# Performance work log

Measured on AMD Instinct MI355X. Metric: run time of the kernel, lower is better.

## Reference

```python
import jax, jax.numpy as jnp
import numpy as np

NUM_EXPERTS = 8
EMBED_DIM = 1024
BATCH, SEQ = 4, 2048


def setup_inputs() -> dict:
    key = jax.random.key(0)
    k1, k2, k3 = jax.random.split(key, 3)
    E_symb = jax.random.normal(k1, (BATCH, SEQ, EMBED_DIM), dtype=jnp.float32)
    gate_w = jax.random.normal(k2, (EMBED_DIM, NUM_EXPERTS), dtype=jnp.float32) * 0.02
    gate_b = jnp.zeros((NUM_EXPERTS,), dtype=jnp.float32)
    expert_w = jax.random.normal(k3, (NUM_EXPERTS, EMBED_DIM, EMBED_DIM), dtype=jnp.float32) * 0.02
    return {"E_symb": E_symb, "gate_w": gate_w, "gate_b": gate_b,
            "expert_w": expert_w, "k": 2}


def reference(E_symb, gate_w, gate_b, expert_w, k):
    B, S, D = E_symb.shape
    E = expert_w.shape[0]
    x = E_symb.reshape(-1, D)                       # [T, D]
    logits = x @ gate_w + gate_b                    # [T, E]
    probs = jax.nn.softmax(logits.astype(jnp.float32), axis=-1)
    # top-k selection; NOTE: original renormalizes routing_weights but never
    # applies them to expert outputs -> combine is an UNWEIGHTED sum.
    _, sel = jax.lax.top_k(probs, k)                # [T, k]
    mask = jax.nn.one_hot(sel, E, dtype=x.dtype).sum(axis=1)  # [T, E] in {0,1}
    # dense grouped-GEMM then masked combine (replaces per-expert gather/scatter loop)
    y = jnp.einsum('td,edf->tef', x, expert_w)      # [T, E, D]
    out = jnp.einsum('tef,te->tf', y, mask)         # [T, D]
    return out.reshape(B, S, D)
```

## Files before the change

kernel.cpp:

```cpp
#include <hip/hip_runtime.h>
#include <hip/hip_bf16.h>
#include <stdint.h>

#define T_TOK 8192
#define DIM   1024
#define NEXP  8
#define BM    128
#define BN    128
#define BK    64

typedef __bf16 bf16_t;
typedef bf16_t bf16x8 __attribute__((ext_vector_type(8)));
typedef bf16_t bf16x4 __attribute__((ext_vector_type(4)));
typedef float  f32x4  __attribute__((ext_vector_type(4)));

#define WS_CNT    0
#define CIDX(p)   ((p) << 4)
#define WS_LIST   8192
#define WS_XBF    (4u << 20)
#define WS_W2     (20u << 20)
#define WS_NEED_PSUM ((size_t)76 << 20)

__device__ const int d_PA[28] = {0,0,0,0,0,0,0,1,1,1,1,1,1,2,2,2,2,2,3,3,3,3,4,4,4,5,5,6};
__device__ const int d_PB[28] = {1,2,3,4,5,6,7,2,3,4,5,6,7,3,4,5,6,7,4,5,6,7,5,6,7,6,7,7};

__device__ __forceinline__ void gload16(const void* g, void* l) {
    __builtin_amdgcn_global_load_lds(
        (const __attribute__((address_space(1))) unsigned int*)g,
        (__attribute__((address_space(3))) unsigned int*)l, 16, 0, 0);
}

__device__ __forceinline__ int swz(int r, int k) {
    return ((r * BK + k) * 2) ^ ((r & 7) << 4);
}

#define WAITCNT_VM0()   do { asm volatile("s_waitcnt vmcnt(0)" ::: "memory"); \
                             __builtin_amdgcn_sched_barrier(0); } while (0)
#define WAITCNT_VM8()   do { asm volatile("s_waitcnt vmcnt(8)" ::: "memory"); \
                             __builtin_amdgcn_sched_barrier(0); } while (0)
#define WAITCNT_LGKM0() do { asm volatile("s_waitcnt lgkmcnt(0)" ::: "memory"); \
                             __builtin_amdgcn_sched_barrier(0); } while (0)
#define BARRIER()       do { __builtin_amdgcn_s_barrier(); \
                             __builtin_amdgcn_sched_barrier(0); } while (0)

template <int PSUM>
__global__ __launch_bounds__(256) void fused_pre(const float* __restrict__ x,
                                                 const float* __restrict__ gw,
                                                 const float* __restrict__ gb,
                                                 const float* __restrict__ ew,
                                                 bf16_t* __restrict__ xbf,
                                                 bf16_t* __restrict__ w2,
                                                 int* __restrict__ cnt,
                                                 int* __restrict__ list) {
    __shared__ __align__(16) float sh[NEXP * DIM];
    int bx  = blockIdx.x;
    int tid = threadIdx.x;
    if (bx < 1024) {
        float4 gb0 = *(const float4*)gb;
        float4 gb1 = *(const float4*)(gb + 4);
        float gbl[8] = {gb0.x, gb0.y, gb0.z, gb0.w, gb1.x, gb1.y, gb1.z, gb1.w};
        float* gwt = sh;
        const float4* gw4 = (const float4*)gw;
        #pragma unroll
        for (int i = 0; i < 8; i++) {
            int f4 = tid + i * 256;
            float4 v = gw4[f4];
            int d  = f4 >> 1;
            int e0 = (f4 & 1) * 4;
            gwt[(e0 + 0) * DIM + d] = v.x;
            gwt[(e0 + 1) * DIM + d] = v.y;
            gwt[(e0 + 2) * DIM + d] = v.z;
            gwt[(e0 + 3) * DIM + d] = v.w;
        }
        __syncthreads();
        int wid  = tid >> 6;
        int lane = tid & 63;
        const float4* gwt4 = (const float4*)gwt;
        for (int tt = 0; tt < 2; tt++) {
            int t = bx * 8 + wid * 2 + tt;
            const float4* xr4 = (const float4*)(x + (size_t)t * DIM);
            float acc[NEXP] = {};
            #pragma unroll
            for (int j = 0; j < 4; j++) {
                int c4 = j * 64 + lane;
                float4 v = xr4[c4];
                bf16x4 b;
                b[0] = (bf16_t)v.x; b[1] = (bf16_t)v.y;
                b[2] = (bf16_t)v.z; b[3] = (bf16_t)v.w;
                *(bf16x4*)(xbf + (size_t)t * DIM + c4 * 4) = b;
                #pragma unroll
                for (int e = 0; e < NEXP; e++) {
                    float4 g = gwt4[e * 256 + c4];
                    acc[e] += v.x * g.x + v.y * g.y + v.z * g.z + v.w * g.w;
                }
            }
            for (int off = 32; off >= 1; off >>= 1)
                #pragma unroll
                for (int e = 0; e < NEXP; e++)
                    acc[e] += __shfl_xor(acc[e], off, 64);
            if (lane == 0) {
                float logit[NEXP];
                #pragma unroll
                for (int e = 0; e < NEXP; e++) logit[e] = acc[e] + gbl[e];
                int b1 = 0; float best = logit[0];
                for (int e = 1; e < NEXP; e++) if (logit[e] > best) { best = logit[e]; b1 = e; }
                int b2 = -1; float best2 = -3.0e38f;
                for (int e = 0; e < NEXP; e++) {
                    if (e == b1) continue;
                    if (logit[e] > best2) { best2 = logit[e]; b2 = e; }
                }
                int a = min(b1, b2), bb = max(b1, b2);
                int p = a * 8 + bb;
                int pos = atomicAdd(&cnt[CIDX(p)], 1);
                list[p * T_TOK + pos] = t;
            }
        }
    } else {
        int bz  = bx - 1024;
        int g   = bz >> 8;
        int rem = bz & 255;
        int f0  = (rem & 15) * 64;
        int d0  = (rem >> 4) * 64;
        float (*tile)[65] = (float (*)[65])sh;
        int a = PSUM ? d_PA[g] : g;
        int b = PSUM ? d_PB[g] : g;
        const float* s1 = ew + ((size_t)a * DIM + d0) * DIM + f0;
        const float* s2 = ew + ((size_t)b * DIM + d0) * DIM + f0;
        int fl = (tid & 15) * 4;
        int dl = tid >> 4;
        #pragma unroll
        for (int i = 0; i < 4; i++) {
            int d = dl + i * 16;
            float4 u = *(const float4*)(s1 + (size_t)d * DIM + fl);
            if (PSUM) {
                float4 v = *(const float4*)(s2 + (size_t)d * DIM + fl);
                u.x += v.x; u.y += v.y; u.z += v.z; u.w += v.w;
            }
            tile[d][fl + 0] = u.x; tile[d][fl + 1] = u.y;
            tile[d][fl + 2] = u.z; tile[d][fl + 3] = u.w;
        }
        __syncthreads();
        bf16_t* dst = w2 + ((size_t)g * DIM + f0) * DIM + d0;
        int dl2 = (tid & 7) * 8;
        int fl2 = tid >> 3;
        #pragma unroll
        for (int i = 0; i < 2; i++) {
            int f = fl2 + i * 32;
            bf16x8 o;
            #pragma unroll
            for (int c = 0; c < 8; c++) o[c] = (bf16_t)tile[dl2 + c][f];
            *(bf16x8*)(dst + (size_t)f * DIM + dl2) = o;
        }
    }
}

template <int PSUM>
__global__ __launch_bounds__(256, 2) void moe_gemm(const bf16_t* __restrict__ xbf,
                                                   const bf16_t* __restrict__ wsrc,
                                                   const int* __restrict__ cnt,
                                                   const int* __restrict__ list,
                                                   float* __restrict__ out) {
    __shared__ __align__(16) bf16_t As[2][BM * BK];
    __shared__ __align__(16) bf16_t Bs[2][BN * BK];
    __shared__ int toks[BM];
    __shared__ int s_desc[128];
    __shared__ int s_ntile;
    int tid  = threadIdx.x;
    int lane = tid & 63;
    int wv   = tid >> 6;
    int wm   = wv >> 1, wn = wv & 1;

    if (tid < 64) {
        int c  = cnt[CIDX(tid)];
        int tp = (c + BM - 1) >> 7;
        int pre = 0, tot = 0;
        for (int i = 0; i < 64; i++) {
            int v = __shfl(tp, i, 64);
            if (i < tid) pre += v;
            tot += v;
        }
        for (int j = 0; j < tp; j++)
            s_desc[pre + j] = tid | ((j * BM) << 8);
        if (tid == 0) s_ntile = tot;
    }
    __syncthreads();
    int nwork = s_ntile * (DIM / BN);
    int vb = ((blockIdx.x & 7) << 6) | (blockIdx.x >> 3);

    for (int wi = 0; wi < 2; wi++) {
        int w = vb * 2 + wi;
        if (w >= nwork) break;
        __syncthreads();
        int dsc = s_desc[w >> 3];
        int n0  = (w & 7) * BN;
        int p   = dsc & 63;
        int m0  = dsc >> 8;
        int e1  = p >> 3, e2 = p & 7;
        int cp  = cnt[CIDX(p)];
        int valid = min(BM, cp - m0);
        if (tid < BM) toks[tid] = list[p * T_TOK + m0 + min(tid, valid - 1)];
        __syncthreads();

        const bf16_t* asrc[4];
        #pragma unroll
        for (int i = 0; i < 4; i++) {
            int c = i * 256 + tid;
            int r = c >> 3, js = (c & 7) ^ (r & 7);
            asrc[i] = xbf + (size_t)toks[r] * DIM + js * 8;
        }

        f32x4 acc[4][4] = {};
        int lr = lane & 15;
        int lk = (lane >> 4) * 8;

        if (PSUM) {
            const bf16_t* bsrc[4];
            int pk = e1 * 7 - (e1 * (e1 - 1)) / 2 + (e2 - e1 - 1);
            const bf16_t* bb = wsrc + (size_t)pk * DIM * DIM;
            #pragma unroll
            for (int i = 0; i < 4; i++) {
                int c = i * 256 + tid;
                int r = c >> 3, js = (c & 7) ^ (r & 7);
                bsrc[i] = bb + (size_t)(n0 + r) * DIM + js * 8;
            }
            #pragma unroll
            for (int i = 0; i < 4; i++)
                gload16(asrc[i], &As[0][(i * 256 + wv * 64) * 8]);
            #pragma unroll
            for (int i = 0; i < 4; i++)
                gload16(bsrc[i], &Bs[0][(i * 256 + wv * 64) * 8]);

            for (int ks = 0; ks < DIM / BK; ks++) {
                int cur = ks & 1;
                if (ks < DIM / BK - 1) {
                    int k1 = (ks + 1) * BK;
                    #pragma unroll
                    for (int i = 0; i < 4; i++)
                        gload16(asrc[i] + k1, &As[cur ^ 1][(i * 256 + wv * 64) * 8]);
                    #pragma unroll
                    for (int i = 0; i < 4; i++)
                        gload16(bsrc[i] + k1, &Bs[cur ^ 1][(i * 256 + wv * 64) * 8]);
                    WAITCNT_VM8();
                } else {
                    WAITCNT_VM0();
                }
                BARRIER();
                const char* Ab = (const char*)As[cur];
                const char* Bb = (const char*)Bs[cur];
                bf16x8 af[2][4], bfr[2][4];
                #pragma unroll
                for (int kk = 0; kk < 2; kk++) {
                    #pragma unroll
                    for (int mf = 0; mf < 4; mf++)
                        af[kk][mf] = *(const bf16x8*)(Ab + swz(wm * 64 + mf * 16 + lr, kk * 32 + lk));
                    #pragma unroll
                    for (int nf = 0; nf < 4; nf++)
                        bfr[kk][nf] = *(const bf16x8*)(Bb + swz(wn * 64 + nf * 16 + lr, kk * 32 + lk));
                }
                #pragma unroll
                for (int kk = 0; kk < 2; kk++)
                    #pragma unroll
                    for (int mf = 0; mf < 4; mf++)
                        #pragma unroll
                        for (int nf = 0; nf < 4; nf++)
                            acc[mf][nf] = __builtin_amdgcn_mfma_f32_16x16x32_bf16(
                                af[kk][mf], bfr[kk][nf], acc[mf][nf], 0, 0, 0);
                BARRIER();
            }
        } else {
            const bf16_t* wt1 = wsrc + (size_t)e1 * DIM * DIM;
            const bf16_t* wt2 = wsrc + (size_t)e2 * DIM * DIM;
            for (int ks = 0; ks < DIM / BK; ks++) {
                int k0 = ks * BK;
                #pragma unroll
                for (int i = 0; i < 4; i++)
                    gload16(asrc[i] + k0, &As[0][(i * 256 + wv * 64) * 8]);
                #pragma unroll
                for (int fo = 0; fo < 2; fo++) {
                    int f = fo * 64 + (tid >> 2), q = tid & 3;
                    const bf16_t* s1 = wt1 + (size_t)(n0 + f) * DIM + k0 + q * 16;
                    const bf16_t* s2 = wt2 + (size_t)(n0 + f) * DIM + k0 + q * 16;
                    bf16x8 u0 = *(const bf16x8*)s1, u1 = *(const bf16x8*)(s1 + 8);
                    bf16x8 w0 = *(const bf16x8*)s2, w1 = *(const bf16x8*)(s2 + 8);
                    bf16x8 o0, o1;
                    #pragma unroll
                    for (int i = 0; i < 8; i++) {
                        o0[i] = (bf16_t)((float)u0[i] + (float)w0[i]);
                        o1[i] = (bf16_t)((float)u1[i] + (float)w1[i]);
                    }
                    *(bf16x8*)((char*)Bs[0] + swz(f, q * 16))     = o0;
                    *(bf16x8*)((char*)Bs[0] + swz(f, q * 16 + 8)) = o1;
                }
                WAITCNT_LGKM0();
                WAITCNT_VM0();
                BARRIER();
                const char* Ab = (const char*)As[0];
                const char* Bb = (const char*)Bs[0];
                bf16x8 af[2][4], bfr[2][4];
                #pragma unroll
                for (int kk = 0; kk < 2; kk++) {
                    #pragma unroll
                    for (int mf = 0; mf < 4; mf++)
                        af[kk][mf] = *(const bf16x8*)(Ab + swz(wm * 64 + mf * 16 + lr, kk * 32 + lk));
                    #pragma unroll
                    for (int nf = 0; nf < 4; nf++)
                        bfr[kk][nf] = *(const bf16x8*)(Bb + swz(wn * 64 + nf * 16 + lr, kk * 32 + lk));
                }
                #pragma unroll
                for (int kk = 0; kk < 2; kk++)
                    #pragma unroll
                    for (int mf = 0; mf < 4; mf++)
                        #pragma unroll
                        for (int nf = 0; nf < 4; nf++)
                            acc[mf][nf] = __builtin_amdgcn_mfma_f32_16x16x32_bf16(
                                af[kk][mf], bfr[kk][nf], acc[mf][nf], 0, 0, 0);
                BARRIER();
            }
        }

        #pragma unroll
        for (int mf = 0; mf < 4; mf++) {
            #pragma unroll
            for (int reg = 0; reg < 4; reg++) {
                int rl = wm * 64 + mf * 16 + (lane >> 4) * 4 + reg;
                if (rl < valid) {
                    size_t trow = (size_t)toks[rl] * DIM;
                    #pragma unroll
                    for (int nf = 0; nf < 4; nf++)
                        out[trow + n0 + wn * 64 + nf * 16 + lr] = acc[mf][nf][reg];
                }
            }
        }
    }
}

extern "C" void kernel_launch(void* const* d_in, const int* in_sizes, int n_in,
                              void* d_out, int out_size, void* d_ws, size_t ws_size,
                              hipStream_t stream) {
    const float* x  = (const float*)d_in[0];
    const float* gw = (const float*)d_in[1];
    const float* gb = (const float*)d_in[2];
    const float* ew = (const float*)d_in[3];
    float* out = (float*)d_out;
    char* ws = (char*)d_ws;
    int*    cnt  = (int*)(ws + WS_CNT);
    int*    list = (int*)(ws + WS_LIST);
    bf16_t* xbf  = (bf16_t*)(ws + WS_XBF);
    bf16_t* w2   = (bf16_t*)(ws + WS_W2);
    bool psum = (ws_size >= WS_NEED_PSUM);

    hipMemsetAsync(d_ws, 0, 8192, stream);
    if (psum) {
        fused_pre<1><<<dim3(1024 + 28 * 256), 256, 0, stream>>>(x, gw, gb, ew,
                                                                xbf, w2, cnt, list);
        moe_gemm<1><<<dim3(512), 256, 0, stream>>>(xbf, w2, cnt, list, out);
    } else {
        fused_pre<0><<<dim3(1024 + 8 * 256), 256, 0, stream>>>(x, gw, gb, ew,
                                                               xbf, w2, cnt, list);
        moe_gemm<0><<<dim3(512), 256, 0, stream>>>(xbf, w2, cnt, list, out);
    }
}
```

Before: 82.37 us.

## Halve GEMM K-tile, one tile per block, raise occupancy to four blocks

The grouped MoE GEMM moves from a 64-wide K tile to a 32-wide one, which halves shared memory per block and adjusts the swizzle to match. Launch bounds rise from 2 to 4 blocks per CU. The grid doubles to 1024 blocks, each handling a single output tile instead of looping over two. The aim is more resident waves to hide global-to-LDS latency and better load balance, at the cost of twice as many K iterations with barriers and less MFMA work per barrier.

```diff
diff --git a/kernel.cpp b/kernel.cpp
--- a/kernel.cpp
+++ b/kernel.cpp
@@ -7,7 +7,7 @@
 #define NEXP  8
 #define BM    128
 #define BN    128
-#define BK    64
+#define BK2   32
 
 typedef __bf16 bf16_t;
 typedef bf16_t bf16x8 __attribute__((ext_vector_type(8)));
@@ -30,13 +30,13 @@
         (__attribute__((address_space(3))) unsigned int*)l, 16, 0, 0);
 }
 
-__device__ __forceinline__ int swz(int r, int k) {
-    return ((r * BK + k) * 2) ^ ((r & 7) << 4);
+__device__ __forceinline__ int swz32(int r, int k) {
+    return ((r * BK2 + k) * 2) ^ (((r >> 1) & 3) << 4);
 }
 
 #define WAITCNT_VM0()   do { asm volatile("s_waitcnt vmcnt(0)" ::: "memory"); \
                              __builtin_amdgcn_sched_barrier(0); } while (0)
-#define WAITCNT_VM8()   do { asm volatile("s_waitcnt vmcnt(8)" ::: "memory"); \
+#define WAITCNT_VM4()   do { asm volatile("s_waitcnt vmcnt(4)" ::: "memory"); \
                              __builtin_amdgcn_sched_barrier(0); } while (0)
 #define WAITCNT_LGKM0() do { asm volatile("s_waitcnt lgkmcnt(0)" ::: "memory"); \
                              __builtin_amdgcn_sched_barrier(0); } while (0)
@@ -155,13 +155,13 @@
 }
 
 template <int PSUM>
-__global__ __launch_bounds__(256, 2) void moe_gemm(const bf16_t* __restrict__ xbf,
+__global__ __launch_bounds__(256, 4) void moe_gemm(const bf16_t* __restrict__ xbf,
                                                    const bf16_t* __restrict__ wsrc,
                                                    const int* __restrict__ cnt,
                                                    const int* __restrict__ list,
                                                    float* __restrict__ out) {
-    __shared__ __align__(16) bf16_t As[2][BM * BK];
-    __shared__ __align__(16) bf16_t Bs[2][BN * BK];
+    __shared__ __align__(16) bf16_t As[2][BM * BK2];
+    __shared__ __align__(16) bf16_t Bs[2][BN * BK2];
     __shared__ int toks[BM];
     __shared__ int s_desc[128];
     __shared__ int s_ntile;
@@ -185,150 +185,131 @@
     }
     __syncthreads();
     int nwork = s_ntile * (DIM / BN);
-    int vb = ((blockIdx.x & 7) << 6) | (blockIdx.x >> 3);
-
-    for (int wi = 0; wi < 2; wi++) {
-        int w = vb * 2 + wi;
-        if (w >= nwork) break;
-        __syncthreads();
-        int dsc = s_desc[w >> 3];
-        int n0  = (w & 7) * BN;
-        int p   = dsc & 63;
-        int m0  = dsc >> 8;
-        int e1  = p >> 3, e2 = p & 7;
-        int cp  = cnt[CIDX(p)];
-        int valid = min(BM, cp - m0);
-        if (tid < BM) toks[tid] = list[p * T_TOK + m0 + min(tid, valid - 1)];
-        __syncthreads();
-
-        const bf16_t* asrc[4];
-        #pragma unroll
-        for (int i = 0; i < 4; i++) {
+    int vb = ((blockIdx.x & 7) << 7) | (blockIdx.x >> 3);
+    if (vb >= nwork) return;
+
+    int dsc = s_desc[vb >> 3];
+    int n0  = (vb & 7) * BN;
+    int p   = dsc & 63;
+    int m0  = dsc >> 8;
+    int e1  = p >> 3, e2 = p & 7;
+    int cp  = cnt[CIDX(p)];
+    int valid = min(BM, cp - m0);
+    if (tid < BM) toks[tid] = list[p * T_TOK + m0 + min(tid, valid - 1)];
+    __syncthreads();
+
+    const bf16_t* asrc[2];
+    #pragma unroll
+    for (int i = 0; i < 2; i++) {
+        int c = i * 256 + tid;
+        int r = c >> 2, js = (c & 3) ^ ((r >> 1) & 3);
+        asrc[i] = xbf + (size_t)toks[r] * DIM + js * 8;
+    }
+
+    f32x4 acc[4][4] = {};
+    int lr = lane & 15;
+    int lk = (lane >> 4) * 8;
+
+    if (PSUM) {
+        const bf16_t* bsrc[2];
+        int pk = e1 * 7 - (e1 * (e1 - 1)) / 2 + (e2 - e1 - 1);
+        const bf16_t* bb = wsrc + (size_t)pk * DIM * DIM;
+        #pragma unroll
+        for (int i = 0; i < 2; i++) {
             int c = i * 256 + tid;
-            int r = c >> 3, js = (c & 7) ^ (r & 7);
-            asrc[i] = xbf + (size_t)toks[r] * DIM + js * 8;
-        }
-
-        f32x4 acc[4][4] = {};
-        int lr = lane & 15;
-        int lk = (lane >> 4) * 8;
-
-        if (PSUM) {
-            const bf16_t* bsrc[4];
-            int pk = e1 * 7 - (e1 * (e1 - 1)) / 2 + (e2 - e1 - 1);
-            const bf16_t* bb = wsrc + (size_t)pk * DIM * DIM;
-            #pragma unroll
-            for (int i = 0; i < 4; i++) {
+            int r = c >> 2, js = (c & 3) ^ ((r >> 1) & 3);
+            bsrc[i] = bb + (size_t)(n0 + r) * DIM + js * 8;
+        }
+        #pragma unroll
+        for (int i = 0; i < 2; i++)
+            gload16(asrc[i], &As[0][(i * 256 + wv * 64) * 8]);
+        #pragma unroll
+        for (int i = 0; i < 2; i++)
+            gload16(bsrc[i], &Bs[0][(i * 256 + wv * 64) * 8]);
+
+        for (int ks = 0; ks < DIM / BK2; ks++) {
+            int cur = ks & 1;
+            if (ks < DIM / BK2 - 1) {
+                int k1 = (ks + 1) * BK2;
+                #pragma unroll
+                for (int i = 0; i < 2; i++)
+                    gload16(asrc[i] + k1, &As[cur ^ 1][(i * 256 + wv * 64) * 8]);
+                #pragma unroll
+                for (int i = 0; i < 2; i++)
+                    gload16(bsrc[i] + k1, &Bs[cur ^ 1][(i * 256 + wv * 64) * 8]);
+                WAITCNT_VM4();
+            } else {
+                WAITCNT_VM0();
+            }
+            BARRIER();
+            const char* Ab = (const char*)As[cur];
+            const char* Bb = (const char*)Bs[cur];
+            bf16x8 af[4], bfr[4];
+            #pragma unroll
+            for (int mf = 0; mf < 4; mf++)
+                af[mf] = *(const bf16x8*)(Ab + swz32(wm * 64 + mf * 16 + lr, lk));
+            #pragma unroll
+            for (int nf = 0; nf < 4; nf++)
+                bfr[nf] = *(const bf16x8*)(Bb + swz32(wn * 64 + nf * 16 + lr, lk));
+            #pragma unroll
+            for (int mf = 0; mf < 4; mf++)
+                #pragma unroll
+                for (int nf = 0; nf < 4; nf++)
+                    acc[mf][nf] = __builtin_amdgcn_mfma_f32_16x16x32_bf16(
+                        af[mf], bfr[nf], acc[mf][nf], 0, 0, 0);
+            BARRIER();
+        }
+    } else {
+        const bf16_t* wt1 = wsrc + (size_t)e1 * DIM * DIM;
+        const bf16_t* wt2 = wsrc + (size_t)e2 * DIM * DIM;
+        for (int ks = 0; ks < DIM / BK2; ks++) {
+            int k0 = ks * BK2;
+            #pragma unroll
+            for (int i = 0; i < 2; i++)
+                gload16(asrc[i] + k0, &As[0][(i * 256 + wv * 64) * 8]);
+            #pragma unroll
+            for (int i = 0; i < 2; i++) {
                 int c = i * 256 + tid;
-                int r = c >> 3, js = (c & 7) ^ (r & 7);
-                bsrc[i] = bb + (size_t)(n0 + r) * DIM + js * 8;
-            }
-            #pragma unroll
-            for (int i = 0; i < 4; i++)
-                gload16(asrc[i], &As[0][(i * 256 + wv * 64) * 8]);
-            #pragma unroll
-            for (int i = 0; i < 4; i++)
-                gload16(bsrc[i], &Bs[0][(i * 256 + wv * 64) * 8]);
-
-            for (int ks = 0; ks < DIM / BK; ks++) {
-                int cur = ks & 1;
-                if (ks < DIM / BK - 1) {
-                    int k1 = (ks + 1) * BK;
-                    #pragma unroll
-                    for (int i = 0; i < 4; i++)
-                        gload16(asrc[i] + k1, &As[cur ^ 1][(i * 256 + wv * 64) * 8]);
-                    #pragma unroll
-                    for (int i = 0; i < 4; i++)
-                        gload16(bsrc[i] + k1, &Bs[cur ^ 1][(i * 256 + wv * 64) * 8]);
-                    WAITCNT_VM8();
-                } else {
-                    WAITCNT_VM0();
-                }
-                BARRIER();
-                const char* Ab = (const char*)As[cur];
-                const char* Bb = (const char*)Bs[cur];
-                bf16x8 af[2][4], bfr[2][4];
-                #pragma unroll
-                for (int kk = 0; kk < 2; kk++) {
-                    #pragma unroll
-                    for (int mf = 0; mf < 4; mf++)
-                        af[kk][mf] = *(const bf16x8*)(Ab + swz(wm * 64 + mf * 16 + lr, kk * 32 + lk));
-                    #pragma unroll
-                    for (int nf = 0; nf < 4; nf++)
-                        bfr[kk][nf] = *(const bf16x8*)(Bb + swz(wn * 64 + nf * 16 + lr, kk * 32 + lk));
-                }
-                #pragma unroll
-                for (int kk = 0; kk < 2; kk++)
-                    #pragma unroll
-                    for (int mf = 0; mf < 4; mf++)
-                        #pragma unroll
-                        for (int nf = 0; nf < 4; nf++)
-                            acc[mf][nf] = __builtin_amdgcn_mfma_f32_16x16x32_bf16(
-                                af[kk][mf], bfr[kk][nf], acc[mf][nf], 0, 0, 0);
-                BARRIER();
-            }
-        } else {
-            const bf16_t* wt1 = wsrc + (size_t)e1 * DIM * DIM;
-            const bf16_t* wt2 = wsrc + (size_t)e2 * DIM * DIM;
-            for (int ks = 0; ks < DIM / BK; ks++) {
-                int k0 = ks * BK;
-                #pragma unroll
-                for (int i = 0; i < 4; i++)
-                    gload16(asrc[i] + k0, &As[0][(i * 256 + wv * 64) * 8]);
-                #pragma unroll
-                for (int fo = 0; fo < 2; fo++) {
-                    int f = fo * 64 + (tid >> 2), q = tid & 3;
-                    const bf16_t* s1 = wt1 + (size_t)(n0 + f) * DIM + k0 + q * 16;
-                    const bf16_t* s2 = wt2 + (size_t)(n0 + f) * DIM + k0 + q * 16;
-                    bf16x8 u0 = *(const bf16x8*)s1, u1 = *(const bf16x8*)(s1 + 8);
-                    bf16x8 w0 = *(const bf16x8*)s2, w1 = *(const bf16x8*)(s2 + 8);
-                    bf16x8 o0, o1;
-                    #pragma unroll
-                    for (int i = 0; i < 8; i++) {
-                        o0[i] = (bf16_t)((float)u0[i] + (float)w0[i]);
-                        o1[i] = (bf16_t)((float)u1[i] + (float)w1[i]);
-                    }
-                    *(bf16x8*)((char*)Bs[0] + swz(f, q * 16))     = o0;
-                    *(bf16x8*)((char*)Bs[0] + swz(f, q * 16 + 8)) = o1;
-                }
-                WAITCNT_LGKM0();
-                WAITCNT_VM0();
-                BARRIER();
-                const char* Ab = (const char*)As[0];
-                const char* Bb = (const char*)Bs[0];
-                bf16x8 af[2][4], bfr[2][4];
-                #pragma unroll
-                for (int kk = 0; kk < 2; kk++) {
-                    #pragma unroll
-                    for (int mf = 0; mf < 4; mf++)
-                        af[kk][mf] = *(const bf16x8*)(Ab + swz(wm * 64 + mf * 16 + lr, kk * 32 + lk));
-                    #pragma unroll
-                    for (int nf = 0; nf < 4; nf++)
-                        bfr[kk][nf] = *(const bf16x8*)(Bb + swz(wn * 64 + nf * 16 + lr, kk * 32 + lk));
-                }
-                #pragma unroll
-                for (int kk = 0; kk < 2; kk++)
-                    #pragma unroll
-                    for (int mf = 0; mf < 4; mf++)
-                        #pragma unroll
-                        for (int nf = 0; nf < 4; nf++)
-                            acc[mf][nf] = __builtin_amdgcn_mfma_f32_16x16x32_bf16(
-                                af[kk][mf], bfr[kk][nf], acc[mf][nf], 0, 0, 0);
-                BARRIER();
-            }
-        }
-
-        #pragma unroll
-        for (int mf = 0; mf < 4; mf++) {
-            #pragma unroll
-            for (int reg = 0; reg < 4; reg++) {
-                int rl = wm * 64 + mf * 16 + (lane >> 4) * 4 + reg;
-                if (rl < valid) {
-                    size_t trow = (size_t)toks[rl] * DIM;
-                    #pragma unroll
-                    for (int nf = 0; nf < 4; nf++)
-                        out[trow + n0 + wn * 64 + nf * 16 + lr] = acc[mf][nf][reg];
-                }
+                int f = c >> 2, j = c & 3;
+                const bf16_t* s1 = wt1 + (size_t)(n0 + f) * DIM + k0 + j * 8;
+                const bf16_t* s2 = wt2 + (size_t)(n0 + f) * DIM + k0 + j * 8;
+                bf16x8 u = *(const bf16x8*)s1, w = *(const bf16x8*)s2, o;
+                #pragma unroll
+                for (int q = 0; q < 8; q++) o[q] = (bf16_t)((float)u[q] + (float)w[q]);
+                *(bf16x8*)((char*)Bs[0] + swz32(f, j * 8)) = o;
+            }
+            WAITCNT_LGKM0();
+            WAITCNT_VM0();
+            BARRIER();
+            const char* Ab = (const char*)As[0];
+            const char* Bb = (const char*)Bs[0];
+            bf16x8 af[4], bfr[4];
+            #pragma unroll
+            for (int mf = 0; mf < 4; mf++)
+                af[mf] = *(const bf16x8*)(Ab + swz32(wm * 64 + mf * 16 + lr, lk));
+            #pragma unroll
+            for (int nf = 0; nf < 4; nf++)
+                bfr[nf] = *(const bf16x8*)(Bb + swz32(wn * 64 + nf * 16 + lr, lk));
+            #pragma unroll
+            for (int mf = 0; mf < 4; mf++)
+                #pragma unroll
+                for (int nf = 0; nf < 4; nf++)
+                    acc[mf][nf] = __builtin_amdgcn_mfma_f32_16x16x32_bf16(
+                        af[mf], bfr[nf], acc[mf][nf], 0, 0, 0);
+            BARRIER();
+        }
+    }
+
+    #pragma unroll
+    for (int mf = 0; mf < 4; mf++) {
+        #pragma unroll
+        for (int reg = 0; reg < 4; reg++) {
+            int rl = wm * 64 + mf * 16 + (lane >> 4) * 4 + reg;
+            if (rl < valid) {
+                size_t trow = (size_t)toks[rl] * DIM;
+                #pragma unroll
+                for (int nf = 0; nf < 4; nf++)
+                    out[trow + n0 + wn * 64 + nf * 16 + lr] = acc[mf][nf][reg];
             }
         }
     }
@@ -353,10 +334,10 @@
     if (psum) {
         fused_pre<1><<<dim3(1024 + 28 * 256), 256, 0, stream>>>(x, gw, gb, ew,
                                                                 xbf, w2, cnt, list);
-        moe_gemm<1><<<dim3(512), 256, 0, stream>>>(xbf, w2, cnt, list, out);
+        moe_gemm<1><<<dim3(1024), 256, 0, stream>>>(xbf, w2, cnt, list, out);
     } else {
         fused_pre<0><<<dim3(1024 + 8 * 256), 256, 0, stream>>>(x, gw, gb, ew,
                                                                xbf, w2, cnt, list);
-        moe_gemm<0><<<dim3(512), 256, 0, stream>>>(xbf, w2, cnt, list, out);
-    }
-}
+        moe_gemm<0><<<dim3(1024), 256, 0, stream>>>(xbf, w2, cnt, list, out);
+    }
+}
```

Result: no change. 83.64 us (+1.5%).
